# Optimization experiments

Hardware: AMD Instinct MI355X
Metric: run time of the kernel (lower is better)

## Reference

```python
import jax, jax.numpy as jnp
import numpy as np
from jax.ops import segment_sum

N = 50000
IN_C, HID_C, OUT_C = 128, 128, 64
ALPHA, BETA = 1.0, 0.0


def add_self_loops(edge_index, num_nodes):
    ar = jnp.arange(num_nodes, dtype=edge_index.dtype)
    loops = jnp.stack([ar, ar])  # [2, N]
    return jnp.concatenate([edge_index, loops], axis=1)


def directed_gcn_conv(x, edge_index, W, b, alpha, beta, self_loops=True):
    n = x.shape[0]
    if self_loops:
        edge_index = add_self_loops(edge_index, n)
    x = x @ W.T + b  # [N, out_c]
    row, col = edge_index[0], edge_index[1]
    ones = jnp.ones(row.shape[0], dtype=x.dtype)
    in_degree = segment_sum(ones, col, num_segments=n)
    out_degree = segment_sum(ones, row, num_segments=n)
    in_norm_inv = jnp.power(in_degree, -alpha)
    out_norm_inv = jnp.power(out_degree, -beta)
    norm = in_norm_inv[col] * out_norm_inv[row]  # [E]
    msgs = norm[:, None] * x[row]  # gather + scale: [E, out_c]
    return segment_sum(msgs, col, num_segments=n)  # scatter-add: [N, out_c]


def setup_inputs() -> dict:
    key = jax.random.key(0)
    ks = jax.random.split(key, 6)
    x = jax.random.normal(ks[0], (N, IN_C), dtype=jnp.float32)
    edge_index = jax.random.randint(ks[1], (2, 800000), 0, N, dtype=jnp.int32)
    s1 = 1.0 / np.sqrt(IN_C)
    W1 = jax.random.uniform(ks[2], (HID_C, IN_C), jnp.float32, -s1, s1)
    b1 = jax.random.uniform(ks[3], (HID_C,), jnp.float32, -s1, s1)
    s2 = 1.0 / np.sqrt(HID_C)
    W2 = jax.random.uniform(ks[4], (OUT_C, HID_C), jnp.float32, -s2, s2)
    b2 = jax.random.uniform(ks[5], (OUT_C,), jnp.float32, -s2, s2)
    return {"x": x, "edge_index": edge_index, "W1": W1, "b1": b1, "W2": W2, "b2": b2}


def reference(x, edge_index, W1, b1, W2, b2):
    h = jax.nn.relu(directed_gcn_conv(x, edge_index, W1, b1, ALPHA, BETA, True))
    out = directed_gcn_conv(h, jnp.flip(edge_index, axis=0), W2, b2, ALPHA, BETA, True)
    return out
```

## Files before the change

### kernel.cpp

```cpp
#include <hip/hip_runtime.h>

typedef unsigned int uint32;
typedef unsigned short u16;
typedef unsigned char u8;

typedef __attribute__((ext_vector_type(8))) short short8;
typedef __attribute__((ext_vector_type(4))) float f32x4;

__device__ __forceinline__ float bf16_s(u16 s) {
  uint32 v = ((uint32)s) << 16;
  return __builtin_bit_cast(float, v);
}
__device__ __forceinline__ float bf16_lo(uint32 u) {
  uint32 v = u << 16;
  return __builtin_bit_cast(float, v);
}
__device__ __forceinline__ float bf16_hi(uint32 u) {
  uint32 v = u & 0xffff0000u;
  return __builtin_bit_cast(float, v);
}
__device__ __forceinline__ u16 f2bf(float f) {
  uint32 u = __builtin_bit_cast(uint32, f);
  u += 0x7fffu + ((u >> 16) & 1u);
  return (u16)(u >> 16);
}

__device__ __forceinline__ void acc_fp8x4(f32x4& a, uint32 v) {
#if __has_builtin(__builtin_amdgcn_cvt_pk_f32_fp8)
  auto lo = __builtin_amdgcn_cvt_pk_f32_fp8((int)v, false);
  auto hi = __builtin_amdgcn_cvt_pk_f32_fp8((int)v, true);
  a[0] += lo[0]; a[1] += lo[1]; a[2] += hi[0]; a[3] += hi[1];
#else
  auto dec = [](uint32 u) -> float {
    uint32 s = u >> 7, e = (u >> 3) & 15, m = u & 7;
    float nrm = __builtin_bit_cast(float, (s << 31) | ((e + 120) << 23) | (m << 20));
    float sub = (s ? -1.f : 1.f) * (float)m * (1.f / 512.f);
    return e ? nrm : sub;
  };
  a[0] += dec(v & 0xFF); a[1] += dec((v >> 8) & 0xFF);
  a[2] += dec((v >> 16) & 0xFF); a[3] += dec(v >> 24);
#endif
}
__device__ __forceinline__ u8 f2fp8(float f) {
#if __has_builtin(__builtin_amdgcn_cvt_pk_fp8_f32)
  int p = __builtin_amdgcn_cvt_pk_fp8_f32(f, f, 0, false);
  return (u8)(p & 0xFF);
#else
  uint32 b = __builtin_bit_cast(uint32, f);
  uint32 s = (b >> 31) << 7;
  float a = fabsf(f);
  uint32 ab = b & 0x7fffffffu;
  uint32 r = ab + 0x7FFFFu + ((ab >> 20) & 1u);
  int e8 = (int)(r >> 23) - 120;
  uint32 m = (r >> 20) & 7;
  if (a < 0.015625f) {
    int q = (int)(a * 512.f + 0.5f);
    return (u8)(s | (uint32)q);
  }
  if (e8 > 15 || (e8 == 15 && m == 7)) return (u8)(s | 0x7E);
  return (u8)(s | ((uint32)e8 << 3) | m);
#endif
}

#define KBUK 128
#define NBUK 256
#define ABUF 48
#define BATCH 4096
#define NPBMAX 512
#define CAPB 24576
#define HS 132

__global__ __launch_bounds__(256) void detect_init(const void* __restrict__ x,
                                                   int* __restrict__ flag,
                                                   int* __restrict__ bsizes) {
  __shared__ int cnt;
  if (threadIdx.x == 0) cnt = 0;
  bsizes[threadIdx.x] = 0;
  __syncthreads();
  const u16* p = (const u16*)x;
  int c = 0;
  for (int i = threadIdx.x; i < 4096; i += 256) {
    u16 s = p[i];
    int e = (s >> 7) & 0xFF;
    c += (s == 0 || (e >= 118 && e <= 130)) ? 1 : 0;
  }
  atomicAdd(&cnt, c);
  __syncthreads();
  if (threadIdx.x == 0) *flag = (cnt > 3072) ? 1 : 0;
}

__global__ __launch_bounds__(256) void prep_count(
    const int* __restrict__ rows, const int* __restrict__ cols,
    int* __restrict__ bsizes, int E, int npb, int nCountBlk,
    const void* __restrict__ x, const void* __restrict__ W1,
    const void* __restrict__ b1, const void* __restrict__ W2,
    const void* __restrict__ b2,
    u16* __restrict__ xb, u16* __restrict__ w1b, u16* __restrict__ w2b,
    float* __restrict__ b1f, float* __restrict__ b2f,
    long nx, const int* __restrict__ flag) {
  __shared__ int h[NBUK];
  if ((int)blockIdx.x < nCountBlk) {
    int t = threadIdx.x;
    h[t] = 0;
    __syncthreads();
    int e0 = blockIdx.x * BATCH;
#pragma unroll
    for (int j = 0; j < BATCH / 256; ++j) {
      int e = e0 + j * 256 + t;
      if (e < E) {
        int r = rows[e], c = cols[e];
        atomicAdd(&h[c / npb], 1);
        atomicAdd(&h[KBUK + r / npb], 1);
      }
    }
    __syncthreads();
    if (h[t] > 0) atomicAdd(&bsizes[t], h[t]);
  } else {
    int isbf = *flag;
    long t = (long)((int)blockIdx.x - nCountBlk) * 256 + threadIdx.x;
    long o1 = nx, o2 = o1 + 128 * 128, o3 = o2 + 64 * 128, o4 = o3 + 128, o5 = o4 + 64;
    if (t < o1) {
      if (!isbf) xb[t] = f2bf(((const float*)x)[t]);
    } else if (t < o2) {
      long i = t - o1;
      w1b[i] = isbf ? ((const u16*)W1)[i] : f2bf(((const float*)W1)[i]);
    } else if (t < o3) {
      long i = t - o2;
      w2b[i] = isbf ? ((const u16*)W2)[i] : f2bf(((const float*)W2)[i]);
    } else if (t < o4) {
      long i = t - o3;
      b1f[i] = isbf ? bf16_s(((const u16*)b1)[i]) : ((const float*)b1)[i];
    } else if (t < o5) {
      long i = t - o4;
      b2f[i] = isbf ? bf16_s(((const u16*)b2)[i]) : ((const float*)b2)[i];
    }
  }
}

__global__ __launch_bounds__(256) void bucket_scan(
    const int* __restrict__ bsizes, int* __restrict__ bbase,
    int* __restrict__ gcur, int* __restrict__ offsets, int ntot) {
  __shared__ int s[NBUK];
  int t = threadIdx.x;
  int v = bsizes[t];
  s[t] = v;
  __syncthreads();
  for (int off = 1; off < 256; off <<= 1) {
    int x = (t >= off) ? s[t - off] : 0;
    __syncthreads();
    s[t] += x;
    __syncthreads();
  }
  int excl = s[t] - v;
  bbase[t] = excl;
  gcur[t] = excl;
  if (t == 255) {
    bbase[NBUK] = s[255];
    offsets[ntot] = s[255];
  }
}

__global__ __launch_bounds__(256) void gemm1_fill(
    const int* __restrict__ rows, const int* __restrict__ cols,
    int* __restrict__ gcur, uint32* __restrict__ gbuf, int E, int npb,
    int nFillBlk,
    const u16* __restrict__ Xdirect, const u16* __restrict__ Xconv,
    const u16* __restrict__ W, const float* __restrict__ Bias,
    u8* __restrict__ Y, int nrows, const int* __restrict__ flag) {
  __shared__ int lcnt[NBUK];
  __shared__ int fbase[NBUK];
  __shared__ uint32 lbuf[NBUK * ABUF];
  if ((int)blockIdx.x < nFillBlk) {
    int t = threadIdx.x;
    lcnt[t] = 0;
    __syncthreads();
    int e0 = blockIdx.x * BATCH;
#pragma unroll
    for (int j = 0; j < BATCH / 256; ++j) {
      int e = e0 + j * 256 + t;
      if (e < E) {
        int r = rows[e], c = cols[e];
        int bk1 = c / npb;
        uint32 en1 = ((uint32)(c - bk1 * npb) << 20) | (uint32)r;
        int p = atomicAdd(&lcnt[bk1], 1);
        if (p < ABUF) lbuf[bk1 * ABUF + p] = en1;
        else { int g = atomicAdd(&gcur[bk1], 1); gbuf[g] = en1; }
        int b2r = r / npb;
        int bk2 = KBUK + b2r;
        uint32 en2 = ((uint32)(r - b2r * npb) << 20) | (uint32)c;
        p = atomicAdd(&lcnt[bk2], 1);
        if (p < ABUF) lbuf[bk2 * ABUF + p] = en2;
        else { int g = atomicAdd(&gcur[bk2], 1); gbuf[g] = en2; }
      }
    }
    __syncthreads();
    int c = min(lcnt[t], ABUF);
    if (c > 0) fbase[t] = atomicAdd(&gcur[t], c);
    __syncthreads();
    int wv = t >> 6, lane = t & 63;
    for (int b = wv * 64; b < wv * 64 + 64; ++b) {
      int cb = min(lcnt[b], ABUF);
      if (cb > 0) {
        int fb = fbase[b];
        for (int jj = lane; jj < cb; jj += 64) gbuf[fb + jj] = lbuf[b * ABUF + jj];
      }
    }
  } else {
    constexpr int NT = 8;
    const u16* X = (*flag) ? Xdirect : Xconv;
    int bid = (int)blockIdx.x - nFillBlk;
    int wave = threadIdx.x >> 6;
    int lane = threadIdx.x & 63;
    int m16 = lane & 15;
    int kq = lane >> 4;
    long rowbase = (long)bid * 64 + wave * 16;
    long arow = rowbase + m16;
    if (arow >= nrows) arow = nrows - 1;
    f32x4 acc[NT];
#pragma unroll
    for (int nt = 0; nt < NT; ++nt) {
      float bv = Bias[nt * 16 + m16];
      acc[nt] = {bv, bv, bv, bv};
    }
#pragma unroll
    for (int ks = 0; ks < 4; ++ks) {
      short8 a = *(const short8*)(X + arow * 128 + ks * 32 + kq * 8);
#pragma unroll
      for (int nt = 0; nt < NT; ++nt) {
        short8 b = *(const short8*)(W + (long)(nt * 16 + m16) * 128 + ks * 32 + kq * 8);
        acc[nt] = __builtin_amdgcn_mfma_f32_16x16x32_bf16(a, b, acc[nt], 0, 0, 0);
      }
    }
    long orow0 = rowbase + kq * 4;
#pragma unroll
    for (int nt = 0; nt < NT; ++nt) {
      int col = nt * 16 + m16;
#pragma unroll
      for (int r = 0; r < 4; ++r) {
        long row = orow0 + r;
        if (row < nrows) Y[row * 128 + col] = f2fp8(acc[nt][r]);
      }
    }
  }
}

__global__ __launch_bounds__(256) void csr_bucket(
    const uint32* __restrict__ gbuf, const int* __restrict__ bbase,
    int* __restrict__ offsets, int* __restrict__ idx, int N, int npb) {
  __shared__ int cnt[NPBMAX];
  __shared__ int s[NPBMAX];
  __shared__ int cur[NPBMAX];
  __shared__ int idxbuf[CAPB];
  int b = blockIdx.x;
  int t = threadIdx.x;
  int csr2 = (b >= KBUK) ? 1 : 0;
  int nb = csr2 ? b - KBUK : b;
  int base_node = nb * npb;
  int nn = N - base_node;
  if (nn > npb) nn = npb;
  if (nn < 0) nn = 0;
  int ebase = bbase[b];
  int ecnt = bbase[b + 1] - ebase;

  cnt[t] = 0; cnt[256 + t] = 0;
  cur[t] = 0; cur[256 + t] = 0;
  __syncthreads();
  for (int i = t; i < ecnt; i += 256)
    atomicAdd(&cnt[gbuf[ebase + i] >> 20], 1);
  __syncthreads();
  s[t] = cnt[t]; s[256 + t] = cnt[256 + t];
  __syncthreads();
  for (int off = 1; off < 256; off <<= 1) {
    int x0 = (t >= off) ? s[t - off] : 0;
    int x1 = (t >= off) ? s[256 + t - off] : 0;
    __syncthreads();
    s[t] += x0; s[256 + t] += x1;
    __syncthreads();
  }
  int h0 = s[255];
  __syncthreads();
  s[256 + t] += h0;
  __syncthreads();
  int obase = csr2 ? N : 0;
  for (int i = t; i < nn; i += 256)
    offsets[obase + base_node + i] = ebase + (s[i] - cnt[i]);
  bool inlds = (ecnt <= CAPB);
  __syncthreads();
  for (int i = t; i < ecnt; i += 256) {
    uint32 en = gbuf[ebase + i];
    int d = en >> 20;
    int src = (int)(en & 0xFFFFFu);
    int p = atomicAdd(&cur[d], 1);
    int pos = (s[d] - cnt[d]) + p;
    if (inlds) idxbuf[pos] = src;
    else idx[ebase + pos] = src;
  }
  __syncthreads();
  if (inlds)
    for (int i = t; i < ecnt; i += 256) idx[ebase + i] = idxbuf[i];
}

__global__ __launch_bounds__(256) void agg1_gemm2(
    const uint32* __restrict__ X,
    const int* __restrict__ idx,
    const int* __restrict__ offsets, const u16* __restrict__ W2,
    const float* __restrict__ Bias2, u16* __restrict__ Y2, int N, int twoE) {
  __shared__ float hl[16 * HS];
  int wv = threadIdx.x >> 6;
  int lane = threadIdx.x & 63;
  int half = lane >> 5;
  int wl = lane & 31;
  int d0 = blockIdx.x * 16;
  unsigned Nm1 = (unsigned)N - 1u;
  for (int rr = 0; rr < 4; ++rr) {
    int row = wv * 4 + rr;
    int d = d0 + row;
    int dl = min(d, N - 1);
    int beg = offsets[dl], end = offsets[dl + 1];
    if (d >= N) { beg = 0; end = 0; }
    int cntv = end - beg;
    if (beg < 0) beg = 0;
    if (end > twoE) end = twoE;
    if (end < beg) { end = beg; cntv = 0; }
    f32x4 p0 = {0, 0, 0, 0}, p1 = {0, 0, 0, 0};
    f32x4 p2 = {0, 0, 0, 0}, p3 = {0, 0, 0, 0};
    int i = beg;
    for (; i + 16 <= end; i += 16) {
      unsigned e0 = min((unsigned)idx[i + half], Nm1);
      unsigned e1 = min((unsigned)idx[i + 2 + half], Nm1);
      unsigned e2 = min((unsigned)idx[i + 4 + half], Nm1);
      unsigned e3 = min((unsigned)idx[i + 6 + half], Nm1);
      unsigned e4 = min((unsigned)idx[i + 8 + half], Nm1);
      unsigned e5 = min((unsigned)idx[i + 10 + half], Nm1);
      unsigned e6 = min((unsigned)idx[i + 12 + half], Nm1);
      unsigned e7 = min((unsigned)idx[i + 14 + half], Nm1);
      uint32 u0 = X[(long)e0 * 32 + wl];
      uint32 u1 = X[(long)e1 * 32 + wl];
      uint32 u2 = X[(long)e2 * 32 + wl];
      uint32 u3 = X[(long)e3 * 32 + wl];
      uint32 u4 = X[(long)e4 * 32 + wl];
      uint32 u5 = X[(long)e5 * 32 + wl];
      uint32 u6 = X[(long)e6 * 32 + wl];
      uint32 u7 = X[(long)e7 * 32 + wl];
      acc_fp8x4(p0, u0); acc_fp8x4(p1, u1);
      acc_fp8x4(p2, u2); acc_fp8x4(p3, u3);
      acc_fp8x4(p0, u4); acc_fp8x4(p1, u5);
      acc_fp8x4(p2, u6); acc_fp8x4(p3, u7);
    }
    for (; i + 2 <= end; i += 2) {
      unsigned e = min((unsigned)idx[i + half], Nm1);
      acc_fp8x4(p0, X[(long)e * 32 + wl]);
    }
    if (half == 0) {
      if (i < end) {
        unsigned e = min((unsigned)idx[i], Nm1);
        acc_fp8x4(p1, X[(long)e * 32 + wl]);
      }
      acc_fp8x4(p2, X[(long)dl * 32 + wl]);
    }
    f32x4 t4 = (p0 + p1) + (p2 + p3);
#pragma unroll
    for (int j = 0; j < 4; ++j) t4[j] += __shfl_xor(t4[j], 32);
    if (half == 0) {
      float s = 1.0f / (float)(cntv + 1);
#pragma unroll
      for (int j = 0; j < 4; ++j)
        hl[row * HS + 4 * wl + j] = fmaxf(t4[j] * s, 0.f);
    }
  }
  __syncthreads();
  int m16 = lane & 15;
  int kq = lane >> 4;
  float bv = Bias2[wv * 16 + m16];
  f32x4 acc = {bv, bv, bv, bv};
#pragma unroll
  for (int ks = 0; ks < 4; ++ks) {
    short8 a;
#pragma unroll
    for (int j = 0; j < 8; ++j)
      a[j] = (short)f2bf(hl[m16 * HS + ks * 32 + kq * 8 + j]);
    short8 b = *(const short8*)(W2 + (long)(wv * 16 + m16) * 128 + ks * 32 + kq * 8);
    acc = __builtin_amdgcn_mfma_f32_16x16x32_bf16(a, b, acc, 0, 0, 0);
  }
  int col = wv * 16 + m16;
#pragma unroll
  for (int r = 0; r < 4; ++r) {
    int row = kq * 4 + r;
    int dd = d0 + row;
    if (dd < N) Y2[(long)dd * 64 + col] = f2bf(acc[r]);
  }
}

__global__ __launch_bounds__(256) void agg2(
    const uint32* __restrict__ Y2w, const int* __restrict__ idx,
    const int* __restrict__ offsets, void* __restrict__ OUT,
    const int* __restrict__ flag, int N, int twoE) {
  int w = (blockIdx.x * 256 + threadIdx.x) >> 6;
  int lane = threadIdx.x & 63;
  int half = lane >> 5;
  int wl = lane & 31;
  if (w >= N) return;
  int beg = offsets[N + w], end = offsets[N + w + 1];
  int cnt = end - beg;
  if (beg < 0) beg = 0;
  if (end > twoE) end = twoE;
  if (end < beg) end = beg;
  unsigned Nm1 = (unsigned)N - 1u;
  float a0 = 0.f, a1 = 0.f, b0 = 0.f, b1 = 0.f;
  float c0 = 0.f, c1 = 0.f, d0 = 0.f, d1 = 0.f;
  int i = beg;
  for (; i + 16 <= end; i += 16) {
    unsigned e0 = min((unsigned)idx[i + half], Nm1);
    unsigned e1 = min((unsigned)idx[i + 2 + half], Nm1);
    unsigned e2 = min((unsigned)idx[i + 4 + half], Nm1);
    unsigned e3 = min((unsigned)idx[i + 6 + half], Nm1);
    unsigned e4 = min((unsigned)idx[i + 8 + half], Nm1);
    unsigned e5 = min((unsigned)idx[i + 10 + half], Nm1);
    unsigned e6 = min((unsigned)idx[i + 12 + half], Nm1);
    unsigned e7 = min((unsigned)idx[i + 14 + half], Nm1);
    uint32 u0 = Y2w[(long)e0 * 32 + wl];
    uint32 u1 = Y2w[(long)e1 * 32 + wl];
    uint32 u2 = Y2w[(long)e2 * 32 + wl];
    uint32 u3 = Y2w[(long)e3 * 32 + wl];
    uint32 u4 = Y2w[(long)e4 * 32 + wl];
    uint32 u5 = Y2w[(long)e5 * 32 + wl];
    uint32 u6 = Y2w[(long)e6 * 32 + wl];
    uint32 u7 = Y2w[(long)e7 * 32 + wl];
    a0 += bf16_lo(u0); a1 += bf16_hi(u0);
    b0 += bf16_lo(u1); b1 += bf16_hi(u1);
    c0 += bf16_lo(u2); c1 += bf16_hi(u2);
    d0 += bf16_lo(u3); d1 += bf16_hi(u3);
    a0 += bf16_lo(u4); a1 += bf16_hi(u4);
    b0 += bf16_lo(u5); b1 += bf16_hi(u5);
    c0 += bf16_lo(u6); c1 += bf16_hi(u6);
    d0 += bf16_lo(u7); d1 += bf16_hi(u7);
  }
  for (; i + 2 <= end; i += 2) {
    unsigned e = min((unsigned)idx[i + half], Nm1);
    uint32 u = Y2w[(long)e * 32 + wl];
    a0 += bf16_lo(u); a1 += bf16_hi(u);
  }
  if (half == 0) {
    if (i < end) {
      unsigned e = min((unsigned)idx[i], Nm1);
      uint32 u = Y2w[(long)e * 32 + wl];
      b0 += bf16_lo(u); b1 += bf16_hi(u);
    }
    uint32 u = Y2w[(long)w * 32 + wl];
    c0 += bf16_lo(u); c1 += bf16_hi(u);
  }
  float t0 = (a0 + b0) + (c0 + d0);
  float t1 = (a1 + b1) + (c1 + d1);
  t0 += __shfl_xor(t0, 32);
  t1 += __shfl_xor(t1, 32);
  if (half == 0) {
    float s = 1.0f / (float)(cnt + 1);
    float m0 = t0 * s, m1 = t1 * s;
    if (*flag)
      ((uint32*)OUT)[(long)w * 32 + wl] = (uint32)f2bf(m0) | ((uint32)f2bf(m1) << 16);
    else
      ((float2*)OUT)[(long)w * 32 + wl] = make_float2(m0, m1);
  }
}


extern "C" void kernel_launch(void* const* d_in, const int* in_sizes, int n_in,
                              void* d_out, int out_size, void* d_ws, size_t ws_size,
                              hipStream_t stream) {
  const void* x  = d_in[0];
  const int* ei  = (const int*)d_in[1];
  const void* W1 = d_in[2];
  const void* b1 = d_in[3];
  const void* W2 = d_in[4];
  const void* b2 = d_in[5];

  int N = in_sizes[0] / 128;
  int E = in_sizes[1] / 2;
  const int* rows = ei;
  const int* cols = ei + E;

  int ntot = 2 * N;
  int npb = (N + KBUK - 1) / KBUK;
  if (npb > NPBMAX || N >= (1 << 20)) return;

  size_t o = 0;
  auto take = [&](size_t bytes) -> void* {
    void* p = (char*)d_ws + o;
    o += (bytes + 255) & ~(size_t)255;
    return p;
  };
  int* flag    = (int*)take(4);
  int* bsizes  = (int*)take(NBUK * 4);
  int* bbase   = (int*)take((NBUK + 1) * 4);
  int* gcur    = (int*)take(NBUK * 4);
  int* offsets = (int*)take((size_t)(ntot + 1) * 4);
  int* idx     = (int*)take((size_t)2 * E * 4);
  uint32* gbuf = (uint32*)take((size_t)2 * E * 4);
  u16* xb      = (u16*)take((size_t)N * 128 * 2);
  u16* w1b     = (u16*)take((size_t)128 * 128 * 2);
  u16* w2b     = (u16*)take((size_t)64 * 128 * 2);
  float* b1f   = (float*)take(128 * 4);
  float* b2f   = (float*)take(64 * 4);
  u8* y1       = (u8*)take((size_t)N * 128);
  u16* y2      = (u16*)take((size_t)N * 64 * 2);

  if (o > ws_size) return;

  long nprep = (long)N * 128 + 128 * 128 + 64 * 128 + 128 + 64;
  int nEblk = (E + BATCH - 1) / BATCH;
  int nPblk = (int)((nprep + 255) / 256);
  int nGblk = (N + 63) / 64;

  detect_init<<<1, 256, 0, stream>>>(x, flag, bsizes);
  prep_count<<<nEblk + nPblk, 256, 0, stream>>>(
      rows, cols, bsizes, E, npb, nEblk,
      x, W1, b1, W2, b2, xb, w1b, w2b, b1f, b2f, (long)N * 128, flag);
  bucket_scan<<<1, 256, 0, stream>>>(bsizes, bbase, gcur, offsets, ntot);
  gemm1_fill<<<nEblk + nGblk, 256, 0, stream>>>(
      rows, cols, gcur, gbuf, E, npb, nEblk,
      (const u16*)x, xb, w1b, b1f, y1, N, flag);
  csr_bucket<<<NBUK, 256, 0, stream>>>(gbuf, bbase, offsets, idx, N, npb);
  agg1_gemm2<<<(N + 15) / 16, 256, 0, stream>>>(
      (const uint32*)y1, idx, offsets, w2b, b2f, y2, N, 2 * E);
  agg2<<<(N + 3) / 4, 256, 0, stream>>>(
      (const uint32*)y2, idx, offsets, d_out, flag, N, 2 * E);
}
```

Baseline: 217.1 us.

## Give each destination row its own wave in agg1_gemm2 and predicate gather tails

agg1_gemm2 now launches 1024 threads per block so each of the 16 destination rows gets its own wave, instead of 4 waves each looping over 4 rows serially. Only the first 4 waves then run the MFMA GEMM. Both aggregation kernels replace the unrolled main loop plus scalar tail loops with one 16-edge predicated loop that clamps index reads and zeroes out-of-range loads. This exposes more memory-level parallelism for the gather and removes tail branches, at the cost of wasted loads on short rows, 12 waves idling during the GEMM, and more pressure from larger blocks.

```diff
diff --git a/kernel.cpp b/kernel.cpp
--- a/kernel.cpp
+++ b/kernel.cpp
@@ -300,7 +300,7 @@
     for (int i = t; i < ecnt; i += 256) idx[ebase + i] = idxbuf[i];
 }
 
-__global__ __launch_bounds__(256) void agg1_gemm2(
+__global__ __launch_bounds__(1024) void agg1_gemm2(
     const uint32* __restrict__ X,
     const int* __restrict__ idx,
     const int* __restrict__ offsets, const u16* __restrict__ W2,
@@ -312,82 +312,61 @@
   int wl = lane & 31;
   int d0 = blockIdx.x * 16;
   unsigned Nm1 = (unsigned)N - 1u;
-  for (int rr = 0; rr < 4; ++rr) {
-    int row = wv * 4 + rr;
-    int d = d0 + row;
-    int dl = min(d, N - 1);
-    int beg = offsets[dl], end = offsets[dl + 1];
-    if (d >= N) { beg = 0; end = 0; }
-    int cntv = end - beg;
-    if (beg < 0) beg = 0;
-    if (end > twoE) end = twoE;
-    if (end < beg) { end = beg; cntv = 0; }
-    f32x4 p0 = {0, 0, 0, 0}, p1 = {0, 0, 0, 0};
-    f32x4 p2 = {0, 0, 0, 0}, p3 = {0, 0, 0, 0};
-    int i = beg;
-    for (; i + 16 <= end; i += 16) {
-      unsigned e0 = min((unsigned)idx[i + half], Nm1);
-      unsigned e1 = min((unsigned)idx[i + 2 + half], Nm1);
-      unsigned e2 = min((unsigned)idx[i + 4 + half], Nm1);
-      unsigned e3 = min((unsigned)idx[i + 6 + half], Nm1);
-      unsigned e4 = min((unsigned)idx[i + 8 + half], Nm1);
-      unsigned e5 = min((unsigned)idx[i + 10 + half], Nm1);
-      unsigned e6 = min((unsigned)idx[i + 12 + half], Nm1);
-      unsigned e7 = min((unsigned)idx[i + 14 + half], Nm1);
-      uint32 u0 = X[(long)e0 * 32 + wl];
-      uint32 u1 = X[(long)e1 * 32 + wl];
-      uint32 u2 = X[(long)e2 * 32 + wl];
-      uint32 u3 = X[(long)e3 * 32 + wl];
-      uint32 u4 = X[(long)e4 * 32 + wl];
-      uint32 u5 = X[(long)e5 * 32 + wl];
-      uint32 u6 = X[(long)e6 * 32 + wl];
-      uint32 u7 = X[(long)e7 * 32 + wl];
-      acc_fp8x4(p0, u0); acc_fp8x4(p1, u1);
-      acc_fp8x4(p2, u2); acc_fp8x4(p3, u3);
-      acc_fp8x4(p0, u4); acc_fp8x4(p1, u5);
-      acc_fp8x4(p2, u6); acc_fp8x4(p3, u7);
-    }
-    for (; i + 2 <= end; i += 2) {
-      unsigned e = min((unsigned)idx[i + half], Nm1);
-      acc_fp8x4(p0, X[(long)e * 32 + wl]);
-    }
-    if (half == 0) {
-      if (i < end) {
-        unsigned e = min((unsigned)idx[i], Nm1);
-        acc_fp8x4(p1, X[(long)e * 32 + wl]);
-      }
-      acc_fp8x4(p2, X[(long)dl * 32 + wl]);
-    }
-    f32x4 t4 = (p0 + p1) + (p2 + p3);
-#pragma unroll
-    for (int j = 0; j < 4; ++j) t4[j] += __shfl_xor(t4[j], 32);
-    if (half == 0) {
-      float s = 1.0f / (float)(cntv + 1);
-#pragma unroll
-      for (int j = 0; j < 4; ++j)
-        hl[row * HS + 4 * wl + j] = fmaxf(t4[j] * s, 0.f);
-    }
-  }
-  __syncthreads();
-  int m16 = lane & 15;
-  int kq = lane >> 4;
-  float bv = Bias2[wv * 16 + m16];
-  f32x4 acc = {bv, bv, bv, bv};
-#pragma unroll
-  for (int ks = 0; ks < 4; ++ks) {
-    short8 a;
-#pragma unroll
-    for (int j = 0; j < 8; ++j)
-      a[j] = (short)f2bf(hl[m16 * HS + ks * 32 + kq * 8 + j]);
-    short8 b = *(const short8*)(W2 + (long)(wv * 16 + m16) * 128 + ks * 32 + kq * 8);
-    acc = __builtin_amdgcn_mfma_f32_16x16x32_bf16(a, b, acc, 0, 0, 0);
-  }
-  int col = wv * 16 + m16;
-#pragma unroll
-  for (int r = 0; r < 4; ++r) {
-    int row = kq * 4 + r;
-    int dd = d0 + row;
-    if (dd < N) Y2[(long)dd * 64 + col] = f2bf(acc[r]);
+  int d = d0 + wv;
+  int dl = min(d, N - 1);
+  int beg = offsets[dl], end = offsets[dl + 1];
+  if (d >= N) { beg = 0; end = 0; }
+  int cntv = end - beg;
+  if (beg < 0) beg = 0;
+  if (end > twoE) end = twoE;
+  if (end < beg) { end = beg; cntv = 0; }
+  f32x4 p0 = {0, 0, 0, 0}, p1 = {0, 0, 0, 0};
+  f32x4 p2 = {0, 0, 0, 0}, p3 = {0, 0, 0, 0};
+  int em1 = (end > beg) ? end - 1 : 0;
+  for (int i = beg; i < end; i += 16) {
+#define LOADJ(k, acc)                                              \
+    {                                                              \
+      int pos = i + 2 * (k) + half;                                \
+      unsigned e = min((unsigned)idx[min(pos, em1)], Nm1);         \
+      uint32 u = (pos < end) ? X[(long)e * 32 + wl] : 0u;          \
+      acc_fp8x4(acc, u);                                           \
+    }
+    LOADJ(0, p0) LOADJ(1, p1) LOADJ(2, p2) LOADJ(3, p3)
+    LOADJ(4, p0) LOADJ(5, p1) LOADJ(6, p2) LOADJ(7, p3)
+#undef LOADJ
+  }
+  if (half == 0) acc_fp8x4(p2, X[(long)dl * 32 + wl]);
+  f32x4 t4 = (p0 + p1) + (p2 + p3);
+#pragma unroll
+  for (int j = 0; j < 4; ++j) t4[j] += __shfl_xor(t4[j], 32);
+  if (half == 0) {
+    float s = (d < N) ? 1.0f / (float)(cntv + 1) : 0.0f;
+#pragma unroll
+    for (int j = 0; j < 4; ++j)
+      hl[wv * HS + 4 * wl + j] = fmaxf(t4[j] * s, 0.f);
+  }
+  __syncthreads();
+  if (wv < 4) {
+    int m16 = lane & 15;
+    int kq = lane >> 4;
+    float bv = Bias2[wv * 16 + m16];
+    f32x4 acc = {bv, bv, bv, bv};
+#pragma unroll
+    for (int ks = 0; ks < 4; ++ks) {
+      short8 a;
+#pragma unroll
+      for (int j = 0; j < 8; ++j)
+        a[j] = (short)f2bf(hl[m16 * HS + ks * 32 + kq * 8 + j]);
+      short8 b = *(const short8*)(W2 + (long)(wv * 16 + m16) * 128 + ks * 32 + kq * 8);
+      acc = __builtin_amdgcn_mfma_f32_16x16x32_bf16(a, b, acc, 0, 0, 0);
+    }
+    int col = wv * 16 + m16;
+#pragma unroll
+    for (int r = 0; r < 4; ++r) {
+      int row = kq * 4 + r;
+      int dd = d0 + row;
+      if (dd < N) Y2[(long)dd * 64 + col] = f2bf(acc[r]);
+    }
   }
 }
 
@@ -408,44 +387,20 @@
   unsigned Nm1 = (unsigned)N - 1u;
   float a0 = 0.f, a1 = 0.f, b0 = 0.f, b1 = 0.f;
   float c0 = 0.f, c1 = 0.f, d0 = 0.f, d1 = 0.f;
-  int i = beg;
-  for (; i + 16 <= end; i += 16) {
-    unsigned e0 = min((unsigned)idx[i + half], Nm1);
-    unsigned e1 = min((unsigned)idx[i + 2 + half], Nm1);
-    unsigned e2 = min((unsigned)idx[i + 4 + half], Nm1);
-    unsigned e3 = min((unsigned)idx[i + 6 + half], Nm1);
-    unsigned e4 = min((unsigned)idx[i + 8 + half], Nm1);
-    unsigned e5 = min((unsigned)idx[i + 10 + half], Nm1);
-    unsigned e6 = min((unsigned)idx[i + 12 + half], Nm1);
-    unsigned e7 = min((unsigned)idx[i + 14 + half], Nm1);
-    uint32 u0 = Y2w[(long)e0 * 32 + wl];
-    uint32 u1 = Y2w[(long)e1 * 32 + wl];
-    uint32 u2 = Y2w[(long)e2 * 32 + wl];
-    uint32 u3 = Y2w[(long)e3 * 32 + wl];
-    uint32 u4 = Y2w[(long)e4 * 32 + wl];
-    uint32 u5 = Y2w[(long)e5 * 32 + wl];
-    uint32 u6 = Y2w[(long)e6 * 32 + wl];
-    uint32 u7 = Y2w[(long)e7 * 32 + wl];
-    a0 += bf16_lo(u0); a1 += bf16_hi(u0);
-    b0 += bf16_lo(u1); b1 += bf16_hi(u1);
-    c0 += bf16_lo(u2); c1 += bf16_hi(u2);
-    d0 += bf16_lo(u3); d1 += bf16_hi(u3);
-    a0 += bf16_lo(u4); a1 += bf16_hi(u4);
-    b0 += bf16_lo(u5); b1 += bf16_hi(u5);
-    c0 += bf16_lo(u6); c1 += bf16_hi(u6);
-    d0 += bf16_lo(u7); d1 += bf16_hi(u7);
-  }
-  for (; i + 2 <= end; i += 2) {
-    unsigned e = min((unsigned)idx[i + half], Nm1);
-    uint32 u = Y2w[(long)e * 32 + wl];
-    a0 += bf16_lo(u); a1 += bf16_hi(u);
+  int em1 = (end > beg) ? end - 1 : 0;
+  for (int i = beg; i < end; i += 16) {
+#define LOADJ2(k, alo, ahi)                                        \
+    {                                                              \
+      int pos = i + 2 * (k) + half;                                \
+      unsigned e = min((unsigned)idx[min(pos, em1)], Nm1);         \
+      uint32 u = (pos < end) ? Y2w[(long)e * 32 + wl] : 0u;        \
+      alo += bf16_lo(u); ahi += bf16_hi(u);                        \
+    }
+    LOADJ2(0, a0, a1) LOADJ2(1, b0, b1) LOADJ2(2, c0, c1) LOADJ2(3, d0, d1)
+    LOADJ2(4, a0, a1) LOADJ2(5, b0, b1) LOADJ2(6, c0, c1) LOADJ2(7, d0, d1)
+#undef LOADJ2
   }
   if (half == 0) {
-    if (i < end) {
-      unsigned e = min((unsigned)idx[i], Nm1);
-      uint32 u = Y2w[(long)e * 32 + wl];
-      b0 += bf16_lo(u); b1 += bf16_hi(u);
-    }
     uint32 u = Y2w[(long)w * 32 + wl];
     c0 += bf16_lo(u); c1 += bf16_hi(u);
   }
@@ -520,7 +475,7 @@
       rows, cols, gcur, gbuf, E, npb, nEblk,
       (const u16*)x, xb, w1b, b1f, y1, N, flag);
   csr_bucket<<<NBUK, 256, 0, stream>>>(gbuf, bbase, offsets, idx, N, npb);
-  agg1_gemm2<<<(N + 15) / 16, 256, 0, stream>>>(
+  agg1_gemm2<<<(N + 15) / 16, 1024, 0, stream>>>(
       (const uint32*)y1, idx, offsets, w2b, b2f, y2, N, 2 * E);
   agg2<<<(N + 3) / 4, 256, 0, stream>>>(
       (const uint32*)y2, idx, offsets, d_out, flag, N, 2 * E);
```

New measurement: 222.4 us. +2.4%, slower.
